# Performance work log

Measured on AMD Instinct MI355X. Metric: run time of the kernel, lower is better.

Reference implementation:

```python
import jax, jax.numpy as jnp
import numpy as np

B, S, A = 65536, 376, 17
H1, H2, K = 400, 300, 15
MAX_ACTION = 1.0


def setup_inputs() -> dict:
    key = jax.random.key(0)
    ks = jax.random.split(key, 16)

    def lin(kw, fan_in, fan_out):
        lim = 1.0 / np.sqrt(fan_in)
        k1, k2 = jax.random.split(kw)
        W = jax.random.uniform(k1, (fan_in, fan_out), jnp.float32, -lim, lim)
        b = jax.random.uniform(k2, (fan_out,), jnp.float32, -lim, lim)
        return W, b

    W1, b1 = lin(ks[0], S, H1)
    W2, b2 = lin(ks[1], H1, H2)
    Wmu, bmu = lin(ks[2], H2, A)
    Wlv, blv = lin(ks[3], H2, A)
    Wu, bu = lin(ks[4], H2, K * A)
    Ww, bw = lin(ks[5], H2, K * A)
    Wb, bb = lin(ks[6], H2, K)
    x = jax.random.normal(ks[7], (B, S), jnp.float32)
    eps = jax.random.normal(ks[8], (B, A), jnp.float32)
    return dict(x=x, eps=eps, W1=W1, b1=b1, W2=W2, b2=b2, Wmu=Wmu, bmu=bmu,
                Wlv=Wlv, blv=blv, Wu=Wu, bu=bu, Ww=Ww, bw=bw, Wb=Wb, bb=bb)


def _flow_chain(action, u, w, b):
    # u, w: (K, B, A); b: (K, B). Sequential planar flow -> lax.scan over K.
    def step(carry, uwb):
        z, ldj = carry
        u_k, w_k, b_k = uwb
        uw = jnp.sum(w_k * u_k, -1)                       # (B,)
        m_uw = -1.0 + jax.nn.softplus(uw)
        w_norm_sq = jnp.sum(w_k * w_k, -1)
        u_hat = u_k + ((m_uw - uw) / w_norm_sq)[:, None] * w_k  # invertibility reparam
        wzb = jnp.sum(w_k * z, -1) + b_k                  # (B,)
        t = jnp.tanh(wzb)
        z_new = z + u_hat * t[:, None]
        psi_u = jnp.sum(w_k * u_hat, -1) * (1.0 - t * t)  # psi^T u_hat
        ldj_new = ldj + jnp.log(jnp.abs(1.0 + psi_u))
        return (z_new, ldj_new), None

    init = (action, jnp.zeros(action.shape[0], action.dtype))
    (z_fin, ldj), _ = jax.lax.scan(step, init, (u, w, b))
    return z_fin, ldj


def reference(x, eps, W1, b1, W2, b2, Wmu, bmu, Wlv, blv, Wu, bu, Ww, bw, Wb, bb):
    h = jax.nn.relu(x @ W1 + b1)
    h = jax.nn.relu(h @ W2 + b2)
    mu = MAX_ACTION * jnp.tanh(h @ Wmu + bmu)
    log_var = MAX_ACTION * jnp.tanh(h @ Wlv + blv)
    std = jnp.exp(log_var)                 # torch code uses log_var.exp() as the scale
    action = mu + std * eps                # rsample

    u = (h @ Wu + bu).reshape(B, K, A).transpose(1, 0, 2)   # (K, B, A)
    w = (h @ Ww + bw).reshape(B, K, A).transpose(1, 0, 2)   # (K, B, A)
    b = (h @ Wb + bb).T                                      # (K, B)

    final_action, log_det_j = _flow_chain(action, u, w, b)

    # Normal(mu, std).log_prob(action) summed over action dim; (action-mu)/std == eps
    log_2pi = jnp.float32(np.log(2.0 * np.pi))
    log_prob = jnp.sum(-0.5 * eps * eps - log_var - 0.5 * log_2pi, axis=-1)
    log_prob_final = log_prob - log_det_j
    prob_final = jnp.exp(log_prob_final)
    return final_action, prob_final, log_prob_final
```

## Files before the change

kernel.cpp:

```cpp
#include <hip/hip_runtime.h>

typedef unsigned short ushort_t;
typedef unsigned int uint_t;
typedef __bf16 bf16x8 __attribute__((ext_vector_type(8)));
typedef float f32x4 __attribute__((ext_vector_type(4)));

#define B_ROWS 65536

#define KT1 12
#define NT1 30
#define KTC1 15
#define KI2 13
#define NT2 20
#define KTC2 10
#define KI3 10
#define NT3 40
#define LDC3 640

#define SZ1 (NT1 * KT1 * 512)
#define SZ2 (NT2 * KI2 * 512)
#define SZ3 (NT3 * KI3 * 512)

__device__ inline float bf2f(ushort_t u) {
    union { uint_t i; float f; } x; x.i = ((uint_t)u) << 16; return x.f;
}
__device__ inline ushort_t f2bf(float f) {
    uint_t u = __float_as_uint(f);
    return (ushort_t)((u + 0x7FFFu + ((u >> 16) & 1u)) >> 16);
}
__device__ inline uint_t pack2(float a, float b) {
    return (uint_t)f2bf(a) | ((uint_t)f2bf(b) << 16);
}
__device__ inline float fast_tanh(float x) {
    float e = __expf(2.f * x);
    return 1.f - 2.f / (e + 1.f);
}
__device__ inline void gl2lds16(const ushort_t* g, ushort_t* l) {
    __builtin_amdgcn_global_load_lds(
        (const __attribute__((address_space(1))) uint_t*)g,
        (__attribute__((address_space(3))) uint_t*)l, 16, 0, 0);
}

__global__ void pack_kernel(const float* __restrict__ W1, const float* __restrict__ W2,
                            const float* __restrict__ Wmu, const float* __restrict__ Wlv,
                            const float* __restrict__ Wu, const float* __restrict__ Ww,
                            const float* __restrict__ Wb,
                            const float* __restrict__ b1, const float* __restrict__ b2,
                            const float* __restrict__ bmu, const float* __restrict__ blv,
                            const float* __restrict__ bu, const float* __restrict__ bw,
                            const float* __restrict__ bb,
                            ushort_t* __restrict__ W1t, ushort_t* __restrict__ W2t,
                            ushort_t* __restrict__ Wht,
                            float* __restrict__ b1p, float* __restrict__ b2p,
                            float* __restrict__ bHp)
{
    int i = blockIdx.x * 256 + threadIdx.x;
    if (i < SZ1) {
        int t = i >> 9, pos = i & 511;
        int l = pos >> 3, j = pos & 7;
        int n = (t / KT1) * 16 + (l & 15);
        int k = (t % KT1) * 32 + (l >> 4) * 8 + j;
        W1t[i] = (n < 400 && k < 376) ? f2bf(W1[k * 400 + n]) : (ushort_t)0;
    } else if (i < SZ1 + SZ2) {
        int i2 = i - SZ1;
        int t = i2 >> 9, pos = i2 & 511;
        int l = pos >> 3, j = pos & 7;
        int n = (t / KI2) * 16 + (l & 15);
        int k = (t % KI2) * 32 + (l >> 4) * 8 + j;
        W2t[i2] = (n < 300 && k < 400) ? f2bf(W2[k * 300 + n]) : (ushort_t)0;
    } else if (i < SZ1 + SZ2 + SZ3) {
        int i3 = i - SZ1 - SZ2;
        int t = i3 >> 9, pos = i3 & 511;
        int l = pos >> 3, j = pos & 7;
        int n = (t / KI3) * 16 + (l & 15);
        int k = (t % KI3) * 32 + (l >> 4) * 8 + j;
        float v = 0.f;
        if (k < 300) {
            if      (n < 17)  v = Wmu[k * 17 + n];
            else if (n < 34)  v = Wlv[k * 17 + (n - 17)];
            else if (n < 289) v = Wu[k * 255 + (n - 34)];
            else if (n < 544) v = Ww[k * 255 + (n - 289)];
            else if (n < 559) v = Wb[k * 15 + (n - 544)];
        }
        Wht[i3] = f2bf(v);
    } else {
        int j = i - SZ1 - SZ2 - SZ3;
        if (j < 480) {
            b1p[j] = (j < 400) ? b1[j] : 0.f;
        } else if (j < 800) {
            int n = j - 480;
            b2p[n] = (n < 300) ? b2[n] : 0.f;
        } else if (j < 1440) {
            int n = j - 800;
            float v = 0.f;
            if      (n < 17)  v = bmu[n];
            else if (n < 34)  v = blv[n - 17];
            else if (n < 289) v = bu[n - 34];
            else if (n < 544) v = bw[n - 289];
            else if (n < 559) v = bb[n - 544];
            bHp[n] = v;
        }
    }
}

__global__ __launch_bounds__(256)
void cvt_kernel(const float* __restrict__ x, ushort_t* __restrict__ xt, int nUnits)
{
    int U = blockIdx.x * 256 + threadIdx.x;
    if (U >= nUnits) return;
    int t = U >> 6, l = U & 63;
    int rowblk = t / KT1, kblk = t - rowblk * KT1;
    long row = (long)rowblk * 16 + (l & 15);
    int k0 = kblk * 32 + (l >> 4) * 8;
    uint4 o = {0u, 0u, 0u, 0u};
    if (k0 + 8 <= 376) {
        const float4* p = reinterpret_cast<const float4*>(x + row * 376 + k0);
        float4 v0 = p[0], v1 = p[1];
        o.x = pack2(v0.x, v0.y); o.y = pack2(v0.z, v0.w);
        o.z = pack2(v1.x, v1.y); o.w = pack2(v1.z, v1.w);
    }
    reinterpret_cast<uint4*>(xt)[U] = o;
}

template<bool RELU, bool OUT_TILED>
__global__ __launch_bounds__(256)
void gemm_tile(const ushort_t* __restrict__ A, const ushort_t* __restrict__ Bt,
               const float* __restrict__ bias, ushort_t* __restrict__ C,
               int kTA, int kIters, int kTC)
{
    __shared__ ushort_t As[8 * 512];
    __shared__ ushort_t Bs[10 * 512];
    const int tid = threadIdx.x;
    const int lane = tid & 63, wv = tid >> 6;
    const int q = lane >> 4, l16 = lane & 15;
    const int nb0 = blockIdx.x * 10;
    const int rowblk0 = blockIdx.y * 8;

    f32x4 acc[2][10];
    #pragma unroll
    for (int r = 0; r < 2; ++r)
        #pragma unroll
        for (int c = 0; c < 10; ++c)
            acc[r][c] = (f32x4){0.f, 0.f, 0.f, 0.f};

    for (int kt = 0; kt < kIters; ++kt) {
        #pragma unroll
        for (int i = 0; i < 2; ++i) {
            int t = wv * 2 + i;
            gl2lds16(A + (((size_t)(rowblk0 + t) * kTA + kt) << 9) + lane * 8,
                     &As[t << 9]);
        }
        #pragma unroll
        for (int t2 = 0; t2 < 3; ++t2) {
            int t = wv + t2 * 4;
            if (t < 10)
                gl2lds16(Bt + (((size_t)(nb0 + t) * kIters + kt) << 9) + lane * 8,
                         &Bs[t << 9]);
        }
        __syncthreads();

        bf16x8 a0 = __builtin_bit_cast(bf16x8,
            *reinterpret_cast<const uint4*>(&As[((wv * 2 + 0) << 9) + lane * 8]));
        bf16x8 a1 = __builtin_bit_cast(bf16x8,
            *reinterpret_cast<const uint4*>(&As[((wv * 2 + 1) << 9) + lane * 8]));
        #pragma unroll
        for (int c = 0; c < 10; ++c) {
            bf16x8 b = __builtin_bit_cast(bf16x8,
                *reinterpret_cast<const uint4*>(&Bs[(c << 9) + lane * 8]));
            acc[0][c] = __builtin_amdgcn_mfma_f32_16x16x32_bf16(a0, b, acc[0][c], 0, 0, 0);
            acc[1][c] = __builtin_amdgcn_mfma_f32_16x16x32_bf16(a1, b, acc[1][c], 0, 0, 0);
        }
        __syncthreads();
    }

    #pragma unroll
    for (int r = 0; r < 2; ++r) {
        int rowblk = rowblk0 + wv * 2 + r;
        #pragma unroll
        for (int c = 0; c < 10; ++c) {
            int n = (nb0 + c) * 16 + l16;
            float bv = bias[n];
            #pragma unroll
            for (int reg = 0; reg < 4; ++reg) {
                float v = acc[r][c][reg] + bv;
                if (RELU) v = fmaxf(v, 0.f);
                int mrow = q * 4 + reg;
                if (OUT_TILED) {
                    size_t off = (((size_t)rowblk * kTC + (n >> 5)) << 9)
                               + (size_t)(((n >> 3) & 3) * 16 + mrow) * 8 + (n & 7);
                    C[off] = f2bf(v);
                } else {
                    long m = (long)rowblk * 16 + mrow;
                    C[m * (long)kTC + n] = f2bf(v);
                }
            }
        }
    }
}

#define FR 128

__global__ __launch_bounds__(FR)
void flow_kernel(const ushort_t* __restrict__ heads, const float* __restrict__ eps,
                 float* __restrict__ out, int rowBase, int B)
{
    __shared__ float lu[17 * (FR + 1)];
    __shared__ float lw[17 * (FR + 1)];
    __shared__ float le[17 * (FR + 1)];
    __shared__ float lb[FR];
    const int tid = threadIdx.x;
    const long row0 = (long)blockIdx.x * FR;
    const ushort_t* hbase = heads + row0 * LDC3;

    for (int idx = tid; idx < FR * 17; idx += FR) {
        int r = idx / 17, i = idx - r * 17;
        lu[i * (FR + 1) + r] = bf2f(hbase[(long)r * LDC3 + i]);
        lw[i * (FR + 1) + r] = bf2f(hbase[(long)r * LDC3 + 17 + i]);
        le[i * (FR + 1) + r] = eps[row0 * 17 + idx];
    }
    __syncthreads();

    float z[17];
    float lp = 0.f;
    #pragma unroll
    for (int i = 0; i < 17; ++i) {
        float mu = fast_tanh(lu[i * (FR + 1) + tid]);
        float lv = fast_tanh(lw[i * (FR + 1) + tid]);
        float ep = le[i * (FR + 1) + tid];
        z[i] = mu + __expf(lv) * ep;
        lp += -0.5f * ep * ep - lv - 0.918938533f;
    }

    float ldj = 0.f;
    for (int k = 0; k < 15; ++k) {
        __syncthreads();
        for (int idx = tid; idx < FR * 17; idx += FR) {
            int r = idx / 17, i = idx - r * 17;
            long rb = (long)r * LDC3;
            lu[i * (FR + 1) + r] = bf2f(hbase[rb + 34 + k * 17 + i]);
            lw[i * (FR + 1) + r] = bf2f(hbase[rb + 289 + k * 17 + i]);
        }
        lb[tid] = bf2f(hbase[(long)tid * LDC3 + 544 + k]);
        __syncthreads();

        float u[17], w[17];
        float uw = 0.f, w2 = 0.f, wz = 0.f;
        #pragma unroll
        for (int i = 0; i < 17; ++i) {
            u[i] = lu[i * (FR + 1) + tid];
            w[i] = lw[i * (FR + 1) + tid];
            uw += w[i] * u[i];
            w2 += w[i] * w[i];
            wz += w[i] * z[i];
        }
        float sp = (uw > 15.f) ? uw : __logf(1.f + __expf(uw));
        float m = sp - 1.f;
        float coef = (m - uw) / fmaxf(w2, 1e-20f);
        float t = fast_tanh(wz + lb[tid]);
        #pragma unroll
        for (int i = 0; i < 17; ++i)
            z[i] += (u[i] + coef * w[i]) * t;
        float psi = m * (1.f - t * t);
        ldj += __logf(fmaxf(fabsf(1.f + psi), 1e-30f));
    }

    const long g = rowBase + row0 + tid;
    #pragma unroll
    for (int i = 0; i < 17; ++i) out[g * 17 + i] = z[i];
    float lpf = lp - ldj;
    out[(long)B * 17 + g] = __expf(lpf);
    out[(long)B * 18 + g] = lpf;
}

extern "C" void kernel_launch(void* const* d_in, const int* in_sizes, int n_in,
                              void* d_out, int out_size, void* d_ws, size_t ws_size,
                              hipStream_t stream)
{
    const float* x   = (const float*)d_in[0];
    const float* eps = (const float*)d_in[1];
    float* out = (float*)d_out;

    const size_t wUS = (size_t)SZ1 + SZ2 + SZ3;
    const size_t fixedBytes = wUS * 2 + (480 + 320 + 640) * 4;
    int Mc = 2048;
    {
        const int cand[6] = {65536, 32768, 16384, 8192, 4096, 2048};
        for (int i = 0; i < 6; ++i) {
            size_t req = (size_t)cand[i] * 2048 + fixedBytes;
            if (req <= ws_size) { Mc = cand[i]; break; }
        }
    }

    ushort_t* region1 = (ushort_t*)d_ws;
    ushort_t* region2 = region1 + (size_t)Mc * 640;
    ushort_t* W1t = region2 + (size_t)Mc * 384;
    ushort_t* W2t = W1t + SZ1;
    ushort_t* Wht = W2t + SZ2;
    float* b1p = (float*)(Wht + SZ3);
    float* b2p = b1p + 480;
    float* bHp = b2p + 320;

    const int packN = SZ1 + SZ2 + SZ3 + 1440;
    pack_kernel<<<(packN + 255) / 256, 256, 0, stream>>>(
        (const float*)d_in[2],  (const float*)d_in[4],
        (const float*)d_in[6],  (const float*)d_in[8],
        (const float*)d_in[10], (const float*)d_in[12], (const float*)d_in[14],
        (const float*)d_in[3],  (const float*)d_in[5],
        (const float*)d_in[7],  (const float*)d_in[9],
        (const float*)d_in[11], (const float*)d_in[13], (const float*)d_in[15],
        W1t, W2t, Wht, b1p, b2p, bHp);

    const int nChunks = B_ROWS / Mc;
    const int nUnits = Mc * 48;
    for (int c = 0; c < nChunks; ++c) {
        const float* xc = x + (size_t)c * Mc * 376;
        cvt_kernel<<<(nUnits + 255) / 256, 256, 0, stream>>>(xc, region2, nUnits);
        gemm_tile<true, true><<<dim3(3, Mc / 128), 256, 0, stream>>>(
            region2, W1t, b1p, region1, KT1, KT1, KTC1);
        gemm_tile<true, true><<<dim3(2, Mc / 128), 256, 0, stream>>>(
            region1, W2t, b2p, region2, KTC1, KI2, KTC2);
        gemm_tile<false, false><<<dim3(4, Mc / 128), 256, 0, stream>>>(
            region2, Wht, bHp, region1, KTC2, KI3, LDC3);
        flow_kernel<<<Mc / FR, FR, 0, stream>>>(region1, eps + (size_t)c * Mc * 17,
                                                out, c * Mc, B_ROWS);
    }
}
```

Baseline: 375.8 us.

## Write head GEMM output column-major per 128-row block; drop LDS staging in flow

The head GEMM now stores its output transposed in 128-row blocks (feature-major, 560 columns, padding columns skipped), so each flow thread reads its own row with coalesced loads directly from global memory. The flow kernel no longer stages u/w/eps through shared memory with per-step barriers, and the K loop is fully unrolled. Workspace per row shrinks from 640 to 560 columns. In exchange the GEMM epilogue stores are strided 2-byte writes, and the flow kernel uses more registers from the unrolled loads.

```diff
diff --git a/kernel.cpp b/kernel.cpp
--- a/kernel.cpp
+++ b/kernel.cpp
@@ -15,7 +15,6 @@
 #define KTC2 10
 #define KI3 10
 #define NT3 40
-#define LDC3 640
 
 #define SZ1 (NT1 * KT1 * 512)
 #define SZ2 (NT2 * KI2 * 512)
@@ -122,7 +121,7 @@
     reinterpret_cast<uint4*>(xt)[U] = o;
 }
 
-template<bool RELU, bool OUT_TILED>
+template<bool RELU, int OMODE>
 __global__ __launch_bounds__(256)
 void gemm_tile(const ushort_t* __restrict__ A, const ushort_t* __restrict__ Bt,
                const float* __restrict__ bias, ushort_t* __restrict__ C,
@@ -185,70 +184,54 @@
                 float v = acc[r][c][reg] + bv;
                 if (RELU) v = fmaxf(v, 0.f);
                 int mrow = q * 4 + reg;
-                if (OUT_TILED) {
+                if (OMODE == 0) {
                     size_t off = (((size_t)rowblk * kTC + (n >> 5)) << 9)
                                + (size_t)(((n >> 3) & 3) * 16 + mrow) * 8 + (n & 7);
                     C[off] = f2bf(v);
                 } else {
-                    long m = (long)rowblk * 16 + mrow;
-                    C[m * (long)kTC + n] = f2bf(v);
+                    if (n < 560) {
+                        size_t off = (size_t)(rowblk >> 3) * (560 * 128)
+                                   + (size_t)n * 128 + ((rowblk & 7) * 16 + mrow);
+                        C[off] = f2bf(v);
+                    }
                 }
             }
         }
     }
 }
 
-#define FR 128
-
-__global__ __launch_bounds__(FR)
-void flow_kernel(const ushort_t* __restrict__ heads, const float* __restrict__ eps,
+__global__ __launch_bounds__(128)
+void flow_kernel(const ushort_t* __restrict__ hT, const float* __restrict__ eps,
                  float* __restrict__ out, int rowBase, int B)
 {
-    __shared__ float lu[17 * (FR + 1)];
-    __shared__ float lw[17 * (FR + 1)];
-    __shared__ float le[17 * (FR + 1)];
-    __shared__ float lb[FR];
     const int tid = threadIdx.x;
-    const long row0 = (long)blockIdx.x * FR;
-    const ushort_t* hbase = heads + row0 * LDC3;
-
-    for (int idx = tid; idx < FR * 17; idx += FR) {
-        int r = idx / 17, i = idx - r * 17;
-        lu[i * (FR + 1) + r] = bf2f(hbase[(long)r * LDC3 + i]);
-        lw[i * (FR + 1) + r] = bf2f(hbase[(long)r * LDC3 + 17 + i]);
-        le[i * (FR + 1) + r] = eps[row0 * 17 + idx];
-    }
-    __syncthreads();
+    const ushort_t* h = hT + (size_t)blockIdx.x * (560 * 128) + tid;
+    const long g = rowBase + (long)blockIdx.x * 128 + tid;
 
     float z[17];
     float lp = 0.f;
     #pragma unroll
     for (int i = 0; i < 17; ++i) {
-        float mu = fast_tanh(lu[i * (FR + 1) + tid]);
-        float lv = fast_tanh(lw[i * (FR + 1) + tid]);
-        float ep = le[i * (FR + 1) + tid];
+        float mu = fast_tanh(bf2f(h[i * 128]));
+        float lv = fast_tanh(bf2f(h[(17 + i) * 128]));
+        float ep = eps[g * 17 + i];
         z[i] = mu + __expf(lv) * ep;
         lp += -0.5f * ep * ep - lv - 0.918938533f;
     }
 
     float ldj = 0.f;
+    #pragma unroll
     for (int k = 0; k < 15; ++k) {
-        __syncthreads();
-        for (int idx = tid; idx < FR * 17; idx += FR) {
-            int r = idx / 17, i = idx - r * 17;
-            long rb = (long)r * LDC3;
-            lu[i * (FR + 1) + r] = bf2f(hbase[rb + 34 + k * 17 + i]);
-            lw[i * (FR + 1) + r] = bf2f(hbase[rb + 289 + k * 17 + i]);
-        }
-        lb[tid] = bf2f(hbase[(long)tid * LDC3 + 544 + k]);
-        __syncthreads();
-
         float u[17], w[17];
+        #pragma unroll
+        for (int i = 0; i < 17; ++i) {
+            u[i] = bf2f(h[(34 + k * 17 + i) * 128]);
+            w[i] = bf2f(h[(289 + k * 17 + i) * 128]);
+        }
+        float bk = bf2f(h[(544 + k) * 128]);
         float uw = 0.f, w2 = 0.f, wz = 0.f;
         #pragma unroll
         for (int i = 0; i < 17; ++i) {
-            u[i] = lu[i * (FR + 1) + tid];
-            w[i] = lw[i * (FR + 1) + tid];
             uw += w[i] * u[i];
             w2 += w[i] * w[i];
             wz += w[i] * z[i];
@@ -256,7 +239,7 @@
         float sp = (uw > 15.f) ? uw : __logf(1.f + __expf(uw));
         float m = sp - 1.f;
         float coef = (m - uw) / fmaxf(w2, 1e-20f);
-        float t = fast_tanh(wz + lb[tid]);
+        float t = fast_tanh(wz + bk);
         #pragma unroll
         for (int i = 0; i < 17; ++i)
             z[i] += (u[i] + coef * w[i]) * t;
@@ -264,7 +247,6 @@
         ldj += __logf(fmaxf(fabsf(1.f + psi), 1e-30f));
     }
 
-    const long g = rowBase + row0 + tid;
     #pragma unroll
     for (int i = 0; i < 17; ++i) out[g * 17 + i] = z[i];
     float lpf = lp - ldj;
@@ -286,14 +268,14 @@
     {
         const int cand[6] = {65536, 32768, 16384, 8192, 4096, 2048};
         for (int i = 0; i < 6; ++i) {
-            size_t req = (size_t)cand[i] * 2048 + fixedBytes;
+            size_t req = (size_t)cand[i] * 1888 + fixedBytes;
             if (req <= ws_size) { Mc = cand[i]; break; }
         }
     }
 
-    ushort_t* region1 = (ushort_t*)d_ws;
-    ushort_t* region2 = region1 + (size_t)Mc * 640;
-    ushort_t* W1t = region2 + (size_t)Mc * 384;
+    ushort_t* regA = (ushort_t*)d_ws;
+    ushort_t* regB = regA + (size_t)Mc * 384;
+    ushort_t* W1t = regB + (size_t)Mc * 560;
     ushort_t* W2t = W1t + SZ1;
     ushort_t* Wht = W2t + SZ2;
     float* b1p = (float*)(Wht + SZ3);
@@ -314,14 +296,14 @@
     const int nUnits = Mc * 48;
     for (int c = 0; c < nChunks; ++c) {
         const float* xc = x + (size_t)c * Mc * 376;
-        cvt_kernel<<<(nUnits + 255) / 256, 256, 0, stream>>>(xc, region2, nUnits);
-        gemm_tile<true, true><<<dim3(3, Mc / 128), 256, 0, stream>>>(
-            region2, W1t, b1p, region1, KT1, KT1, KTC1);
-        gemm_tile<true, true><<<dim3(2, Mc / 128), 256, 0, stream>>>(
-            region1, W2t, b2p, region2, KTC1, KI2, KTC2);
-        gemm_tile<false, false><<<dim3(4, Mc / 128), 256, 0, stream>>>(
-            region2, Wht, bHp, region1, KTC2, KI3, LDC3);
-        flow_kernel<<<Mc / FR, FR, 0, stream>>>(region1, eps + (size_t)c * Mc * 17,
-                                                out, c * Mc, B_ROWS);
-    }
-}
+        cvt_kernel<<<(nUnits + 255) / 256, 256, 0, stream>>>(xc, regA, nUnits);
+        gemm_tile<true, 0><<<dim3(3, Mc / 128), 256, 0, stream>>>(
+            regA, W1t, b1p, regB, KT1, KT1, KTC1);
+        gemm_tile<true, 0><<<dim3(2, Mc / 128), 256, 0, stream>>>(
+            regB, W2t, b2p, regA, KTC1, KI2, KTC2);
+        gemm_tile<false, 1><<<dim3(4, Mc / 128), 256, 0, stream>>>(
+            regA, Wht, bHp, regB, KTC2, KI3, 0);
+        flow_kernel<<<Mc / 128, 128, 0, stream>>>(regB, eps + (size_t)c * Mc * 17,
+                                                  out, c * Mc, B_ROWS);
+    }
+}
```

New measurement: 390.0 us. 1.04x slower.
